# Kernel tuning notes

Measured on AMD Instinct MI355X. Metric: run time of the kernel, lower is better.

Reference implementation:

```python
import jax, jax.numpy as jnp
import numpy as np
import math

PC_RANGE = (-15.0, -30.0, -2.0, 15.0, 30.0, 2.0)
MAP_THRESH = 0.5
DIS_THRESH = 2.0
LANE_DIV_CLS_IDX = 0
LOSS_WEIGHT = 1.0
PI = math.pi


def setup_inputs() -> dict:
    key = jax.random.key(0)
    k1, k2, k3 = jax.random.split(key, 3)
    B, T, V, P = 2048, 6, 100, 20
    ego_fut_preds = jax.random.normal(k1, (B, T, 2), dtype=jnp.float32)
    lane_preds = jax.random.uniform(k2, (B, V, P, 2), dtype=jnp.float32)
    lane_score_preds = jax.random.uniform(k3, (B, V, 3), dtype=jnp.float32)
    return {"ego_fut_preds": ego_fut_preds, "lane_preds": lane_preds,
            "lane_score_preds": lane_score_preds}


def _plan_map_dir_loss(pred, target, dis_thresh):
    # pred: [B,T,2] displacements, target: [B,V,P,2] map points
    B, T, _ = pred.shape
    P = target.shape[2]
    pred = jnp.cumsum(pred, axis=-2)                         # trajectory [B,T,2]
    traj_dis = jnp.linalg.norm(pred[:, -1] - pred[:, 0], axis=-1)
    static_mask = traj_dis < 1.0                             # [B]

    # nearest map instance per (b, t): min over points, argmin over vectors
    d = jnp.linalg.norm(pred[:, :, None, None, :] - target[:, None, :, :, :], axis=-1)  # [B,T,V,P]
    min_inst = jnp.argmin(jnp.min(d, axis=-1), axis=-1)      # [B,T]
    b_idx = jnp.arange(B)[:, None]
    t_idx = jnp.arange(T)[None, :]
    target_map_inst = target[b_idx, min_inst]                # [B,T,P,2]

    # nearest point on that instance
    d2 = jnp.linalg.norm(pred[:, :, None, :] - target_map_inst, axis=-1)  # [B,T,P]
    min_pts_idxs = jnp.argmin(d2, axis=-1)                   # [B,T]
    min_pts_next_idxs = jnp.where(min_pts_idxs == P - 1, P - 2, min_pts_idxs + 1)

    # trajectory yaw, last segment repeated
    traj_yaw = jnp.arctan2(jnp.diff(pred[..., 1], axis=-1),
                           jnp.diff(pred[..., 0], axis=-1))  # [B,T-1]
    traj_yaw = jnp.concatenate([traj_yaw, traj_yaw[:, -1:]], axis=-1)  # [B,T]

    min_pts = target_map_inst[b_idx, t_idx, min_pts_idxs]          # [B,T,2]
    min_pts_next = target_map_inst[b_idx, t_idx, min_pts_next_idxs]  # [B,T,2]
    dist = jnp.linalg.norm(min_pts - pred, axis=-1)          # [B,T]
    dist_mask = dist > dis_thresh

    lane_yaw = jnp.arctan2(min_pts_next[..., 1] - min_pts[..., 1],
                           min_pts_next[..., 0] - min_pts[..., 0])  # [B,T]

    yd = traj_yaw - lane_yaw
    # sequential angle wraps, exactly as in the torch masked assignments
    yd = jnp.where(yd > PI, yd - PI, yd)
    yd = jnp.where(yd > PI / 2, yd - PI, yd)
    yd = jnp.where(yd < -PI, yd + PI, yd)
    yd = jnp.where(yd < -PI / 2, yd + PI, yd)
    yd = jnp.where(dist_mask, 0.0, yd)
    yd = jnp.where(static_mask[:, None], 0.0, yd)
    return jnp.abs(yd)                                       # [B,T]


def reference(ego_fut_preds, lane_preds, lane_score_preds):
    not_lane_div = lane_score_preds[..., LANE_DIV_CLS_IDX] < MAP_THRESH  # [B,V]
    x0, y0, _, x1, y1, _ = PC_RANGE
    lane = jnp.stack([lane_preds[..., 0] * (x1 - x0) + x0,
                      lane_preds[..., 1] * (y1 - y0) + y0], axis=-1)
    lane = jnp.where(not_lane_div[:, :, None, None], 1e6, lane)
    loss = _plan_map_dir_loss(ego_fut_preds, lane, DIS_THRESH)
    return LOSS_WEIGHT * jnp.mean(loss)
```

## Files before the change

### kernel.cpp

```cpp
#include <hip/hip_runtime.h>
#include <math.h>

#define B_TOT 2048
#define T_N 6
#define V_N 100
#define P_N 20

__global__ __launch_bounds__(128) void pmdl_kernel(
    const float* __restrict__ ego,
    const float* __restrict__ lane,
    const float* __restrict__ score,
    float* __restrict__ partial)
{
    const int b   = blockIdx.x;
    const int tid = threadIdx.x;
    const int wv  = tid >> 6;
    const int ln  = tid & 63;

    const float* e = ego + (size_t)b * (T_N * 2);
    float px[T_N], py[T_N];
    {
        float cx = 0.f, cy = 0.f;
        #pragma unroll
        for (int t = 0; t < T_N; ++t) {
            cx += e[2 * t];
            cy += e[2 * t + 1];
            px[t] = cx; py[t] = cy;
        }
    }
    const float tdx = px[T_N - 1] - px[0];
    const float tdy = py[T_N - 1] - py[0];
    const bool static_mask = sqrtf(tdx * tdx + tdy * tdy) < 1.0f;

    float dmin[T_N];
    #pragma unroll
    for (int t = 0; t < T_N; ++t) dmin[t] = 3.0e38f;

    if (tid < V_N) {
        float m2[T_N];
        #pragma unroll
        for (int t = 0; t < T_N; ++t) m2[t] = 3.0e38f;

        const float sc = score[((size_t)b * V_N + tid) * 3];
        if (sc < 0.5f) {
            #pragma unroll
            for (int t = 0; t < T_N; ++t) {
                float dx = px[t] - 1e6f, dy = py[t] - 1e6f;
                m2[t] = fmaf(dx, dx, dy * dy);
            }
        } else {
            const float4* lp =
                (const float4*)(lane + ((size_t)b * V_N + tid) * (P_N * 2));
            #pragma unroll
            for (int j = 0; j < P_N / 2; ++j) {
                float4 q = lp[j];
                float x0 = fmaf(q.x, 30.f, -15.f);
                float y0 = fmaf(q.y, 60.f, -30.f);
                float x1 = fmaf(q.z, 30.f, -15.f);
                float y1 = fmaf(q.w, 60.f, -30.f);
                #pragma unroll
                for (int t = 0; t < T_N; ++t) {
                    float dx0 = px[t] - x0, dy0 = py[t] - y0;
                    float d0  = fmaf(dx0, dx0, dy0 * dy0);
                    float dx1 = px[t] - x1, dy1 = py[t] - y1;
                    float d1  = fmaf(dx1, dx1, dy1 * dy1);
                    m2[t] = fminf(m2[t], fminf(d0, d1));
                }
            }
        }
        #pragma unroll
        for (int t = 0; t < T_N; ++t) dmin[t] = sqrtf(m2[t]);
    }

    __shared__ float smin[2][T_N];
    __shared__ int   svid[2][T_N];
    #pragma unroll
    for (int t = 0; t < T_N; ++t) {
        float m = dmin[t];
        #pragma unroll
        for (int off = 32; off > 0; off >>= 1)
            m = fminf(m, __shfl_down(m, off, 64));
        m = __shfl(m, 0, 64);
        unsigned long long eq = __ballot(dmin[t] == m);
        if (ln == 0) {
            smin[wv][t] = m;
            svid[wv][t] = (wv << 6) + (__ffsll(eq) - 1);
        }
    }
    __syncthreads();

    if (wv == 0) {
        float loss = 0.f;
        if (ln < T_N) {
            const int t = ln;
            const float m0 = smin[0][t], m1 = smin[1][t];
            const int vsel = (m1 < m0) ? svid[1][t] : svid[0][t];

            const float sc = score[((size_t)b * V_N + vsel) * 3];
            const bool real = !(sc < 0.5f);
            const float* basep = lane + ((size_t)b * V_N + vsel) * (P_N * 2);

            float best = 3.0e38f;
            int   bi   = 0;
            const float4* lp = (const float4*)basep;
            #pragma unroll
            for (int j = 0; j < P_N / 2; ++j) {
                float4 q = lp[j];
                float x0 = real ? fmaf(q.x, 30.f, -15.f) : 1e6f;
                float y0 = real ? fmaf(q.y, 60.f, -30.f) : 1e6f;
                float x1 = real ? fmaf(q.z, 30.f, -15.f) : 1e6f;
                float y1 = real ? fmaf(q.w, 60.f, -30.f) : 1e6f;
                float dx0 = x0 - px[t], dy0 = y0 - py[t];
                float d0  = sqrtf(fmaf(dx0, dx0, dy0 * dy0));
                float dx1 = x1 - px[t], dy1 = y1 - py[t];
                float d1  = sqrtf(fmaf(dx1, dx1, dy1 * dy1));
                if (d0 < best) { best = d0; bi = 2 * j; }
                if (d1 < best) { best = d1; bi = 2 * j + 1; }
            }
            const int ni = (bi == P_N - 1) ? P_N - 2 : bi + 1;

            const float2* lp2 = (const float2*)basep;
            float2 c2 = lp2[bi];
            float2 n2 = lp2[ni];
            float cxp = real ? fmaf(c2.x, 30.f, -15.f) : 1e6f;
            float cyp = real ? fmaf(c2.y, 60.f, -30.f) : 1e6f;
            float nxp = real ? fmaf(n2.x, 30.f, -15.f) : 1e6f;
            float nyp = real ? fmaf(n2.y, 60.f, -30.f) : 1e6f;

            float yawx = (t < T_N - 1) ? (px[t + 1] - px[t])
                                       : (px[T_N - 1] - px[T_N - 2]);
            float yawy = (t < T_N - 1) ? (py[t + 1] - py[t])
                                       : (py[T_N - 1] - py[T_N - 2]);
            float tyaw = atan2f(yawy, yawx);
            float lyaw = atan2f(nyp - cyp, nxp - cxp);

            float yd = tyaw - lyaw;
            const float PIf = 3.14159274101257324f;
            if (yd >  PIf)        yd -= PIf;
            if (yd >  0.5f * PIf) yd -= PIf;
            if (yd < -PIf)        yd += PIf;
            if (yd < -0.5f * PIf) yd += PIf;
            if (best > 2.0f)  yd = 0.f;
            if (static_mask)  yd = 0.f;
            loss = fabsf(yd);
        }
        #pragma unroll
        for (int off = 32; off > 0; off >>= 1)
            loss += __shfl_down(loss, off, 64);
        if (ln == 0) partial[b] = loss;
    }
}

__global__ __launch_bounds__(256) void pmdl_reduce(
    const float* __restrict__ partial,
    float* __restrict__ out)
{
    const int tid = threadIdx.x;
    float s = 0.f;
    #pragma unroll
    for (int i = 0; i < B_TOT / 256; ++i) s += partial[tid + i * 256];
    #pragma unroll
    for (int off = 32; off > 0; off >>= 1) s += __shfl_down(s, off, 64);
    __shared__ float wsum[4];
    if ((tid & 63) == 0) wsum[tid >> 6] = s;
    __syncthreads();
    if (tid == 0) {
        float tot = wsum[0] + wsum[1] + wsum[2] + wsum[3];
        out[0] = tot * (1.0f / (float)(B_TOT * T_N));
    }
}

extern "C" void kernel_launch(void* const* d_in, const int* in_sizes, int n_in,
                              void* d_out, int out_size, void* d_ws, size_t ws_size,
                              hipStream_t stream) {
    const float* ego   = (const float*)d_in[0];
    const float* lane  = (const float*)d_in[1];
    const float* score = (const float*)d_in[2];
    float* partialbuf = (float*)d_ws;
    float* out        = (float*)d_out;

    pmdl_kernel<<<B_TOT, 128, 0, stream>>>(ego, lane, score, partialbuf);
    pmdl_reduce<<<1, 256, 0, stream>>>(partialbuf, out);
}
```

Before: 87.83 us.

## Map one batch per wavefront and drop shared-memory block reduction

Each batch element is now processed by a single 64-lane wavefront, where each lane handles vector ln and also vector 64+ln when that index is below 100. Blocks hold four wavefronts, so four batches run per block. The argmin packs the distance bits and the index into a 64-bit key and reduces it with shuffles, which removes the shared memory and __syncthreads. The cost is more work per lane and less parallelism per batch, while the 28 lanes per block that sat idle on vectors before now do useful work.

```diff
diff --git a/kernel.cpp b/kernel.cpp
--- a/kernel.cpp
+++ b/kernel.cpp
@@ -6,16 +6,15 @@
 #define V_N 100
 #define P_N 20
 
-__global__ __launch_bounds__(128) void pmdl_kernel(
+__global__ __launch_bounds__(256) void pmdl_kernel(
     const float* __restrict__ ego,
     const float* __restrict__ lane,
     const float* __restrict__ score,
     float* __restrict__ partial)
 {
-    const int b   = blockIdx.x;
-    const int tid = threadIdx.x;
-    const int wv  = tid >> 6;
-    const int ln  = tid & 63;
+    const int wv = threadIdx.x >> 6;
+    const int ln = threadIdx.x & 63;
+    const int b  = blockIdx.x * 4 + wv;
 
     const float* e = ego + (size_t)b * (T_N * 2);
     float px[T_N], py[T_N];
@@ -32,25 +31,20 @@
     const float tdy = py[T_N - 1] - py[0];
     const bool static_mask = sqrtf(tdx * tdx + tdy * tdy) < 1.0f;
 
-    float dmin[T_N];
-    #pragma unroll
-    for (int t = 0; t < T_N; ++t) dmin[t] = 3.0e38f;
-
-    if (tid < V_N) {
-        float m2[T_N];
-        #pragma unroll
-        for (int t = 0; t < T_N; ++t) m2[t] = 3.0e38f;
-
-        const float sc = score[((size_t)b * V_N + tid) * 3];
+    float mA2[T_N], mB2[T_N];
+    {
+        const float sc = score[((size_t)b * V_N + ln) * 3];
         if (sc < 0.5f) {
             #pragma unroll
             for (int t = 0; t < T_N; ++t) {
                 float dx = px[t] - 1e6f, dy = py[t] - 1e6f;
-                m2[t] = fmaf(dx, dx, dy * dy);
+                mA2[t] = fmaf(dx, dx, dy * dy);
             }
         } else {
+            #pragma unroll
+            for (int t = 0; t < T_N; ++t) mA2[t] = 3.0e38f;
             const float4* lp =
-                (const float4*)(lane + ((size_t)b * V_N + tid) * (P_N * 2));
+                (const float4*)(lane + ((size_t)b * V_N + ln) * (P_N * 2));
             #pragma unroll
             for (int j = 0; j < P_N / 2; ++j) {
                 float4 q = lp[j];
@@ -64,91 +58,127 @@
                     float d0  = fmaf(dx0, dx0, dy0 * dy0);
                     float dx1 = px[t] - x1, dy1 = py[t] - y1;
                     float d1  = fmaf(dx1, dx1, dy1 * dy1);
-                    m2[t] = fminf(m2[t], fminf(d0, d1));
+                    mA2[t] = fminf(mA2[t], fminf(d0, d1));
                 }
             }
         }
-        #pragma unroll
-        for (int t = 0; t < T_N; ++t) dmin[t] = sqrtf(m2[t]);
-    }
-
-    __shared__ float smin[2][T_N];
-    __shared__ int   svid[2][T_N];
-    #pragma unroll
-    for (int t = 0; t < T_N; ++t) {
-        float m = dmin[t];
-        #pragma unroll
-        for (int off = 32; off > 0; off >>= 1)
-            m = fminf(m, __shfl_down(m, off, 64));
-        m = __shfl(m, 0, 64);
-        unsigned long long eq = __ballot(dmin[t] == m);
-        if (ln == 0) {
-            smin[wv][t] = m;
-            svid[wv][t] = (wv << 6) + (__ffsll(eq) - 1);
-        }
-    }
-    __syncthreads();
-
-    if (wv == 0) {
-        float loss = 0.f;
-        if (ln < T_N) {
-            const int t = ln;
-            const float m0 = smin[0][t], m1 = smin[1][t];
-            const int vsel = (m1 < m0) ? svid[1][t] : svid[0][t];
-
-            const float sc = score[((size_t)b * V_N + vsel) * 3];
-            const bool real = !(sc < 0.5f);
-            const float* basep = lane + ((size_t)b * V_N + vsel) * (P_N * 2);
-
-            float best = 3.0e38f;
-            int   bi   = 0;
-            const float4* lp = (const float4*)basep;
+    }
+    const bool hasB = ln < (V_N - 64);
+    if (hasB) {
+        const int v2 = 64 + ln;
+        const float sc = score[((size_t)b * V_N + v2) * 3];
+        if (sc < 0.5f) {
+            #pragma unroll
+            for (int t = 0; t < T_N; ++t) {
+                float dx = px[t] - 1e6f, dy = py[t] - 1e6f;
+                mB2[t] = fmaf(dx, dx, dy * dy);
+            }
+        } else {
+            #pragma unroll
+            for (int t = 0; t < T_N; ++t) mB2[t] = 3.0e38f;
+            const float4* lp =
+                (const float4*)(lane + ((size_t)b * V_N + v2) * (P_N * 2));
             #pragma unroll
             for (int j = 0; j < P_N / 2; ++j) {
                 float4 q = lp[j];
-                float x0 = real ? fmaf(q.x, 30.f, -15.f) : 1e6f;
-                float y0 = real ? fmaf(q.y, 60.f, -30.f) : 1e6f;
-                float x1 = real ? fmaf(q.z, 30.f, -15.f) : 1e6f;
-                float y1 = real ? fmaf(q.w, 60.f, -30.f) : 1e6f;
-                float dx0 = x0 - px[t], dy0 = y0 - py[t];
-                float d0  = sqrtf(fmaf(dx0, dx0, dy0 * dy0));
-                float dx1 = x1 - px[t], dy1 = y1 - py[t];
-                float d1  = sqrtf(fmaf(dx1, dx1, dy1 * dy1));
-                if (d0 < best) { best = d0; bi = 2 * j; }
-                if (d1 < best) { best = d1; bi = 2 * j + 1; }
-            }
-            const int ni = (bi == P_N - 1) ? P_N - 2 : bi + 1;
-
-            const float2* lp2 = (const float2*)basep;
-            float2 c2 = lp2[bi];
-            float2 n2 = lp2[ni];
-            float cxp = real ? fmaf(c2.x, 30.f, -15.f) : 1e6f;
-            float cyp = real ? fmaf(c2.y, 60.f, -30.f) : 1e6f;
-            float nxp = real ? fmaf(n2.x, 30.f, -15.f) : 1e6f;
-            float nyp = real ? fmaf(n2.y, 60.f, -30.f) : 1e6f;
-
-            float yawx = (t < T_N - 1) ? (px[t + 1] - px[t])
-                                       : (px[T_N - 1] - px[T_N - 2]);
-            float yawy = (t < T_N - 1) ? (py[t + 1] - py[t])
-                                       : (py[T_N - 1] - py[T_N - 2]);
-            float tyaw = atan2f(yawy, yawx);
-            float lyaw = atan2f(nyp - cyp, nxp - cxp);
-
-            float yd = tyaw - lyaw;
-            const float PIf = 3.14159274101257324f;
-            if (yd >  PIf)        yd -= PIf;
-            if (yd >  0.5f * PIf) yd -= PIf;
-            if (yd < -PIf)        yd += PIf;
-            if (yd < -0.5f * PIf) yd += PIf;
-            if (best > 2.0f)  yd = 0.f;
-            if (static_mask)  yd = 0.f;
-            loss = fabsf(yd);
-        }
-        #pragma unroll
-        for (int off = 32; off > 0; off >>= 1)
-            loss += __shfl_down(loss, off, 64);
-        if (ln == 0) partial[b] = loss;
-    }
+                float x0 = fmaf(q.x, 30.f, -15.f);
+                float y0 = fmaf(q.y, 60.f, -30.f);
+                float x1 = fmaf(q.z, 30.f, -15.f);
+                float y1 = fmaf(q.w, 60.f, -30.f);
+                #pragma unroll
+                for (int t = 0; t < T_N; ++t) {
+                    float dx0 = px[t] - x0, dy0 = py[t] - y0;
+                    float d0  = fmaf(dx0, dx0, dy0 * dy0);
+                    float dx1 = px[t] - x1, dy1 = py[t] - y1;
+                    float d1  = fmaf(dx1, dx1, dy1 * dy1);
+                    mB2[t] = fminf(mB2[t], fminf(d0, d1));
+                }
+            }
+        }
+    }
+
+    unsigned vsel_u = 0;
+    #pragma unroll
+    for (int t = 0; t < T_N; ++t) {
+        unsigned long long k =
+            ((unsigned long long)__float_as_uint(sqrtf(mA2[t])) << 32)
+            | (unsigned)ln;
+        if (hasB) {
+            unsigned long long kB =
+                ((unsigned long long)__float_as_uint(sqrtf(mB2[t])) << 32)
+                | (unsigned)(64 + ln);
+            if (kB < k) k = kB;
+        }
+        #pragma unroll
+        for (int off = 32; off > 0; off >>= 1) {
+            unsigned long long o = __shfl_down(k, off, 64);
+            if (o < k) k = o;
+        }
+        k = __shfl(k, 0, 64);
+        if (ln == t) vsel_u = (unsigned)(k & 0xFFFFFFFFu);
+    }
+
+    float loss = 0.f;
+    if (ln < T_N) {
+        float pxt = 0.f, pyt = 0.f, yawx = 0.f, yawy = 0.f;
+        #pragma unroll
+        for (int t = 0; t < T_N; ++t) {
+            if (ln == t) {
+                pxt = px[t]; pyt = py[t];
+                yawx = (t < T_N - 1) ? (px[t + 1] - px[t])
+                                     : (px[T_N - 1] - px[T_N - 2]);
+                yawy = (t < T_N - 1) ? (py[t + 1] - py[t])
+                                     : (py[T_N - 1] - py[T_N - 2]);
+            }
+        }
+        const float sc = score[((size_t)b * V_N + vsel_u) * 3];
+        const bool real = !(sc < 0.5f);
+        const float* basep = lane + ((size_t)b * V_N + vsel_u) * (P_N * 2);
+
+        float best = 3.0e38f;
+        int   bi   = 0;
+        const float4* lp = (const float4*)basep;
+        #pragma unroll
+        for (int j = 0; j < P_N / 2; ++j) {
+            float4 q = lp[j];
+            float x0 = real ? fmaf(q.x, 30.f, -15.f) : 1e6f;
+            float y0 = real ? fmaf(q.y, 60.f, -30.f) : 1e6f;
+            float x1 = real ? fmaf(q.z, 30.f, -15.f) : 1e6f;
+            float y1 = real ? fmaf(q.w, 60.f, -30.f) : 1e6f;
+            float dx0 = x0 - pxt, dy0 = y0 - pyt;
+            float d0  = sqrtf(fmaf(dx0, dx0, dy0 * dy0));
+            float dx1 = x1 - pxt, dy1 = y1 - pyt;
+            float d1  = sqrtf(fmaf(dx1, dx1, dy1 * dy1));
+            if (d0 < best) { best = d0; bi = 2 * j; }
+            if (d1 < best) { best = d1; bi = 2 * j + 1; }
+        }
+        const int ni = (bi == P_N - 1) ? P_N - 2 : bi + 1;
+
+        const float2* lp2 = (const float2*)basep;
+        float2 c2 = lp2[bi];
+        float2 n2 = lp2[ni];
+        float cxp = real ? fmaf(c2.x, 30.f, -15.f) : 1e6f;
+        float cyp = real ? fmaf(c2.y, 60.f, -30.f) : 1e6f;
+        float nxp = real ? fmaf(n2.x, 30.f, -15.f) : 1e6f;
+        float nyp = real ? fmaf(n2.y, 60.f, -30.f) : 1e6f;
+
+        float tyaw = atan2f(yawy, yawx);
+        float lyaw = atan2f(nyp - cyp, nxp - cxp);
+
+        float yd = tyaw - lyaw;
+        const float PIf = 3.14159274101257324f;
+        if (yd >  PIf)        yd -= PIf;
+        if (yd >  0.5f * PIf) yd -= PIf;
+        if (yd < -PIf)        yd += PIf;
+        if (yd < -0.5f * PIf) yd += PIf;
+        if (best > 2.0f)  yd = 0.f;
+        if (static_mask)  yd = 0.f;
+        loss = fabsf(yd);
+    }
+    #pragma unroll
+    for (int off = 32; off > 0; off >>= 1)
+        loss += __shfl_down(loss, off, 64);
+    if (ln == 0) partial[b] = loss;
 }
 
 __global__ __launch_bounds__(256) void pmdl_reduce(
@@ -179,6 +209,6 @@
     float* partialbuf = (float*)d_ws;
     float* out        = (float*)d_out;
 
-    pmdl_kernel<<<B_TOT, 128, 0, stream>>>(ego, lane, score, partialbuf);
+    pmdl_kernel<<<B_TOT / 4, 256, 0, stream>>>(ego, lane, score, partialbuf);
     pmdl_reduce<<<1, 256, 0, stream>>>(partialbuf, out);
 }
```

After: 88.78 us. No clear change (+1.1%).
